# Optimization experiments

Measured on AMD Instinct MI355X. Metric: run time of the kernel, lower is better.

## Reference

```python
import jax, jax.numpy as jnp
import numpy as np

L = 2        # num_layers
B = 2        # batch
C = 256      # d_model
H = 8        # nhead
HD = C // H  # head_dim = 32
T = 16       # time_length
S = 512      # seq_length
DFF = 1024   # dim_feedforward
LIMIT = 25.0 # move_limit
EPS = 1e-5


def _xavier(key, shape):
    fan_in, fan_out = shape[-1], shape[-2]
    lim = np.sqrt(6.0 / (fan_in + fan_out)).astype(np.float32)
    return jax.random.uniform(key, shape, jnp.float32, -lim, lim)


def setup_inputs() -> dict:
    key = jax.random.key(0)
    ks = jax.random.split(key, 16)
    decoder = jax.random.normal(ks[0], (B, C, T, S), jnp.float32)
    encoder = jax.random.normal(ks[1], (B, C, T, S), jnp.float32)
    pos = jax.random.normal(ks[2], (B, C, T, S), jnp.float32)
    # coordinates in a 100-unit box so pairwise distances straddle move_limit=25
    coord = jax.random.uniform(ks[3], (B, T, S, 3), jnp.float32) * 100.0
    mask = jax.random.bernoulli(ks[4], 0.2, (B, T, S))  # True = padded key
    # per-layer params (stacked over L). qkv_proj is a groups=3 1x1 conv == three [C,C] mats.
    Wq = _xavier(ks[5], (L, C, C)); bq = jnp.zeros((L, C), jnp.float32)
    Wk = _xavier(ks[6], (L, C, C)); bk = jnp.zeros((L, C), jnp.float32)
    Wv = _xavier(ks[7], (L, C, C)); bv = jnp.zeros((L, C), jnp.float32)
    Wo = _xavier(ks[8], (L, C, C)); bo = jnp.zeros((L, C), jnp.float32)
    W1 = _xavier(ks[9], (L, DFF, C)); b1 = jnp.zeros((L, DFF), jnp.float32)
    W2 = _xavier(ks[10], (L, C, DFF)); b2 = jnp.zeros((L, C), jnp.float32)
    ln_g = jnp.ones((L, 3, C), jnp.float32)
    ln_b = jnp.zeros((L, 3, C), jnp.float32)
    return dict(decoder=decoder, encoder=encoder, pos=pos, coord=coord, mask=mask,
                Wq=Wq, bq=bq, Wk=Wk, bk=bk, Wv=Wv, bv=bv, Wo=Wo, bo=bo,
                W1=W1, b1=b1, W2=W2, b2=b2, ln_g=ln_g, ln_b=ln_b)


def _layernorm_c(x, g, b):
    # LayerNorm over channel dim of [B,C,T,S]
    m = jnp.mean(x, axis=1, keepdims=True)
    v = jnp.mean((x - m) ** 2, axis=1, keepdims=True)
    xn = (x - m) * jax.lax.rsqrt(v + EPS)
    return xn * g[None, :, None, None] + b[None, :, None, None]


def _proj(W, b, x):  # 1x1 conv == channel matmul on [B,C,T,S]
    return jnp.einsum('oc,bcts->bots', W, x) + b[None, :, None, None]


def _heads(x):  # [B,C,T,S] -> [B,H,T,S,HD]
    return x.reshape(B, H, HD, T, S).transpose(0, 1, 3, 4, 2)


def _dist_attn(x_q, x_k, x_v, coord, mask, Wq, bq, Wk, bk, Wv, bv, Wo, bo):
    q = _heads(_proj(Wq, bq, x_q))
    k = _heads(_proj(Wk, bk, x_k))
    v = _heads(_proj(Wv, bv, x_v))
    logits = jnp.einsum('bhtqd,bhtkd->bhtqk', q, k) / np.sqrt(HD).astype(np.float32)
    d2 = jnp.sum((coord[:, :, :, None, :] - coord[:, :, None, :, :]) ** 2, axis=-1)
    gate = (jnp.sqrt(d2) < LIMIT).astype(logits.dtype)  # [B,T,S,S]
    logits = logits * gate[:, None]
    logits = jnp.where(mask[:, None, :, None, :], jnp.asarray(-9e15, logits.dtype), logits)
    attn = jax.nn.softmax(logits, axis=-1)
    vals = jnp.einsum('bhtqk,bhtkd->bhtqd', attn, v)
    vals = vals.transpose(0, 1, 4, 2, 3).reshape(B, C, T, S)
    return _proj(Wo, bo, vals)


def _forward(decoder, encoder, pos, coord, mask,
             Wq, bq, Wk, bk, Wv, bv, Wo, bo, W1, b1, W2, b2, ln_g, ln_b):
    dec = decoder
    for i in range(L):
        a = lambda xq, xk, xv: _dist_attn(xq, xk, xv, coord, mask,
                                          Wq[i], bq[i], Wk[i], bk[i], Wv[i], bv[i], Wo[i], bo[i])
        # self-attention (queries/keys = norm(dec)+pos)
        src2 = _layernorm_c(dec, ln_g[i, 0], ln_b[i, 0])
        qk = src2 + pos
        dec = dec + a(qk, qk, src2)
        # second block: queries/keys from encoder+pos, values from norm(dec)
        # (the original uses self_attn weights here too)
        src2 = _layernorm_c(dec, ln_g[i, 1], ln_b[i, 1])
        qk = encoder + pos
        dec = dec + a(qk, qk, src2)
        # FFN
        src2 = _layernorm_c(dec, ln_g[i, 2], ln_b[i, 2])
        h = jax.nn.relu(jnp.einsum('fc,bcts->bfts', W1[i], src2) + b1[i][None, :, None, None])
        ff = jnp.einsum('cf,bfts->bcts', W2[i], h) + b2[i][None, :, None, None]
        dec = dec + ff
    return dec


def reference(decoder, encoder, pos, coord, mask,
              Wq, bq, Wk, bk, Wv, bv, Wo, bo, W1, b1, W2, b2, ln_g, ln_b):
    return _forward(decoder, encoder, pos, coord, mask,
                    Wq, bq, Wk, bk, Wv, bv, Wo, bo, W1, b1, W2, b2, ln_g, ln_b)
```

## Files before the change

### kernel.cpp

```cpp
#include <hip/hip_runtime.h>
#include <math.h>

#define L_ 2
#define B_ 2
#define C_ 256
#define H_ 8
#define HD_ 32
#define T_ 16
#define S_ 512
#define DFF_ 1024
#define NTS (T_*S_)
#define NELEM ((size_t)B_*C_*T_*S_)
#define QKM 512

typedef _Float16 half8v __attribute__((ext_vector_type(8)));
typedef _Float16 half4v __attribute__((ext_vector_type(4)));
typedef _Float16 half2v __attribute__((ext_vector_type(2)));
typedef float   float4v __attribute__((ext_vector_type(4)));

union h8u { half8v v; half2v h[4]; };

__global__ void prep_kernel(const float* __restrict__ Wq, const float* __restrict__ Wk,
                            const float* __restrict__ Wv, const float* __restrict__ Wo,
                            const float* __restrict__ W1, const float* __restrict__ W2,
                            const float* __restrict__ bq, const float* __restrict__ bk,
                            _Float16* __restrict__ whqk, _Float16* __restrict__ whv,
                            _Float16* __restrict__ who, _Float16* __restrict__ wh1,
                            _Float16* __restrict__ wh2, float* __restrict__ bqk) {
    int i = blockIdx.x * 256 + threadIdx.x;
    const int NQK = L_*QKM*C_;
    const int NCC = L_*C_*C_;
    const int NFC = L_*DFF_*C_;
    if (i < NQK) {
        int k = i & 255, m = (i >> 8) & 511, l = i >> 17;
        float v = (m < 256) ? Wq[((size_t)l*256 + m)*256 + k]
                            : Wk[((size_t)l*256 + (m-256))*256 + k];
        whqk[i] = (_Float16)v;
        return;
    }
    int j = i - NQK;
    if (j < NCC) { whv[j] = (_Float16)Wv[j]; return; }
    j -= NCC;
    if (j < NCC) { who[j] = (_Float16)Wo[j]; return; }
    j -= NCC;
    if (j < NFC) { wh1[j] = (_Float16)W1[j]; return; }
    j -= NFC;
    if (j < NFC) { wh2[j] = (_Float16)W2[j]; return; }
    j -= NFC;
    if (j < L_*QKM) {
        int c = j & 255, sel = (j >> 8) & 1, l = j >> 9;
        bqk[j] = sel ? bk[l*256 + c] : bq[l*256 + c];
    }
}

template<bool HASPOS>
__global__ __launch_bounds__(256) void ln_t(const float* __restrict__ x,
                                            const float* __restrict__ gam,
                                            const float* __restrict__ bet,
                                            const float* __restrict__ pos,
                                            _Float16* __restrict__ s2,
                                            _Float16* __restrict__ qk) {
    __shared__ float redS[8][32];
    __shared__ float redQ[8][32];
    __shared__ _Float16 tiles[(HASPOS ? 2 : 1) * 32 * 256];
    _Float16* t0 = tiles;
    _Float16* t1 = tiles + 32 * 256;
    int tid = threadIdx.x;
    int nl = tid & 31, cg = tid >> 5;
    int gpos = blockIdx.x * 32;
    int b = gpos >> 13, nb = gpos & 8191;
    const float* xb = x + (size_t)b * C_ * NTS + nb + nl;
    float xv[32], pv[HASPOS ? 32 : 1];
    float sum = 0.f, sq = 0.f;
    #pragma unroll
    for (int j = 0; j < 32; ++j) {
        float v = xb[(size_t)(cg * 32 + j) * NTS];
        xv[j] = v; sum += v; sq += v * v;
    }
    if (HASPOS) {
        const float* pb = pos + (size_t)b * C_ * NTS + nb + nl;
        #pragma unroll
        for (int j = 0; j < 32; ++j) pv[j] = pb[(size_t)(cg * 32 + j) * NTS];
    }
    redS[cg][nl] = sum; redQ[cg][nl] = sq;
    __syncthreads();
    float s = 0.f, q = 0.f;
    #pragma unroll
    for (int g = 0; g < 8; ++g) { s += redS[g][nl]; q += redQ[g][nl]; }
    float mean = s * (1.0f / C_);
    float var  = q * (1.0f / C_) - mean * mean;
    float rstd = rsqrtf(var + 1e-5f);
    #pragma unroll
    for (int jj = 0; jj < 4; ++jj) {
        half8v h0, h1;
        #pragma unroll
        for (int j2 = 0; j2 < 8; ++j2) {
            int j = jj * 8 + j2;
            int c = cg * 32 + j;
            float y = (xv[j] - mean) * rstd * gam[c] + bet[c];
            h0[j2] = (_Float16)y;
            if (HASPOS) h1[j2] = (_Float16)(y + pv[j]);
        }
        int cs = (cg * 4 + jj) ^ nl;
        *(half8v*)(t0 + nl * 256 + cs * 8) = h0;
        if (HASPOS) *(half8v*)(t1 + nl * 256 + cs * 8) = h1;
    }
    __syncthreads();
    #pragma unroll
    for (int it = 0; it < 4; ++it) {
        int chunk = tid + it * 256;
        int row = chunk >> 5, ch = chunk & 31;
        int cs = ch ^ row;
        half8v v0 = *(half8v*)(t0 + row * 256 + cs * 8);
        *(half8v*)(s2 + (size_t)(gpos + row) * C_ + ch * 8) = v0;
        if (HASPOS) {
            half8v v1 = *(half8v*)(t1 + row * 256 + cs * 8);
            *(half8v*)(qk + (size_t)(gpos + row) * C_ + ch * 8) = v1;
        }
    }
}

__global__ __launch_bounds__(256) void addt_kernel(const float* __restrict__ a,
                                                   const float* __restrict__ p,
                                                   _Float16* __restrict__ o) {
    __shared__ _Float16 t0[32 * 256];
    int tid = threadIdx.x;
    int nl = tid & 31, cg = tid >> 5;
    int gpos = blockIdx.x * 32;
    int b = gpos >> 13, nb = gpos & 8191;
    const float* ab = a + (size_t)b * C_ * NTS + nb + nl;
    const float* pb = p + (size_t)b * C_ * NTS + nb + nl;
    float av[32], pv[32];
    #pragma unroll
    for (int j = 0; j < 32; ++j) av[j] = ab[(size_t)(cg * 32 + j) * NTS];
    #pragma unroll
    for (int j = 0; j < 32; ++j) pv[j] = pb[(size_t)(cg * 32 + j) * NTS];
    #pragma unroll
    for (int jj = 0; jj < 4; ++jj) {
        half8v h0;
        #pragma unroll
        for (int j2 = 0; j2 < 8; ++j2) {
            int j = jj * 8 + j2;
            h0[j2] = (_Float16)(av[j] + pv[j]);
        }
        int cs = (cg * 4 + jj) ^ nl;
        *(half8v*)(t0 + nl * 256 + cs * 8) = h0;
    }
    __syncthreads();
    #pragma unroll
    for (int it = 0; it < 4; ++it) {
        int chunk = tid + it * 256;
        int row = chunk >> 5, ch = chunk & 31;
        half8v v0 = *(half8v*)(t0 + row * 256 + (ch ^ row) * 8);
        *(half8v*)(o + (size_t)(gpos + row) * C_ + ch * 8) = v0;
    }
}

template<int MODE>
__global__ __launch_bounds__(256) void gemm_mfma(const _Float16* __restrict__ W,
                                                 const float* __restrict__ bias,
                                                 const _Float16* __restrict__ X,
                                                 const float* __restrict__ src,
                                                 void* __restrict__ Yv, int M, int K) {
    __shared__ _Float16 As[128 * 32];
    __shared__ _Float16 Bs[128 * 32];
    int b  = blockIdx.z;
    int m0 = blockIdx.y * 128;
    int n0 = blockIdx.x * 128;
    const _Float16* Xb = X + (size_t)b * NTS * K;
    int tid = threadIdx.x;
    int wave = tid >> 6, lane = tid & 63;
    int wm = (wave >> 1) * 64, wn = (wave & 1) * 64;
    int r = lane & 15, g = lane >> 4;
    float4v acc[4][4];
    #pragma unroll
    for (int i = 0; i < 4; ++i)
        #pragma unroll
        for (int j = 0; j < 4; ++j) acc[i][j] = (float4v){0.f, 0.f, 0.f, 0.f};

    for (int k0 = 0; k0 < K; k0 += 32) {
        #pragma unroll
        for (int it = 0; it < 2; ++it) {
            int cbase = wave * 64 + it * 256;
            int rowbase = cbase >> 2;
            int row = rowbase + (lane >> 2);
            int ch = (lane & 3) ^ (row & 3);
            const _Float16* ga = W  + (size_t)(m0 + row) * K + k0 + ch * 8;
            const _Float16* gb = Xb + (size_t)(n0 + row) * K + k0 + ch * 8;
            __builtin_amdgcn_global_load_lds(
                (const __attribute__((address_space(1))) void*)ga,
                (__attribute__((address_space(3))) void*)(As + rowbase * 32), 16, 0, 0);
            __builtin_amdgcn_global_load_lds(
                (const __attribute__((address_space(1))) void*)gb,
                (__attribute__((address_space(3))) void*)(Bs + rowbase * 32), 16, 0, 0);
        }
        __syncthreads();
        half8v af[4], bf[4];
        #pragma unroll
        for (int mt = 0; mt < 4; ++mt) {
            int row = wm + mt * 16 + r;
            af[mt] = *(const half8v*)(As + row * 32 + ((g ^ (row & 3)) << 3));
        }
        #pragma unroll
        for (int nt = 0; nt < 4; ++nt) {
            int row = wn + nt * 16 + r;
            bf[nt] = *(const half8v*)(Bs + row * 32 + ((g ^ (row & 3)) << 3));
        }
        #pragma unroll
        for (int mt = 0; mt < 4; ++mt)
            #pragma unroll
            for (int nt = 0; nt < 4; ++nt)
                acc[mt][nt] = __builtin_amdgcn_mfma_f32_16x16x32_f16(af[mt], bf[nt], acc[mt][nt], 0, 0, 0);
        __syncthreads();
    }

    #pragma unroll
    for (int mt = 0; mt < 4; ++mt) {
        int m_base = m0 + wm + mt * 16 + g * 4;
        float bb[4];
        #pragma unroll
        for (int rr = 0; rr < 4; ++rr) bb[rr] = bias[m_base + rr];
        #pragma unroll
        for (int nt = 0; nt < 4; ++nt) {
            int n = n0 + wn + nt * 16 + r;
            if (MODE == 1) {
                float* Yd = (float*)Yv + (size_t)b * M * NTS;
                const float* Sd = src + (size_t)b * M * NTS;
                #pragma unroll
                for (int rr = 0; rr < 4; ++rr) {
                    size_t o = (size_t)(m_base + rr) * NTS + n;
                    Yd[o] = Sd[o] + acc[mt][nt][rr] + bb[rr];
                }
            } else {
                _Float16* Y = (_Float16*)Yv + (size_t)b * NTS * M;
                half4v hv;
                #pragma unroll
                for (int rr = 0; rr < 4; ++rr) {
                    float v = acc[mt][nt][rr] + bb[rr];
                    if (MODE == 2) v = fmaxf(v, 0.f);
                    hv[rr] = (_Float16)v;
                }
                *(half4v*)(Y + (size_t)n * M + m_base) = hv;
            }
        }
    }
}

__global__ __launch_bounds__(256) void gate_kernel(const float* __restrict__ coord,
                                                   const int* __restrict__ mask,
                                                   unsigned long long* __restrict__ gwb,
                                                   int* __restrict__ ucb,
                                                   unsigned long long* __restrict__ umb) {
    int wid  = blockIdx.x * 4 + (threadIdx.x >> 6);
    int lane = threadIdx.x & 63;
    int q  = wid & 511;
    int bt = wid >> 9;
    const float* cb = coord + (size_t)bt * S_ * 3;
    const int* mrow = mask + (size_t)bt * S_;
    float cq0 = cb[q*3+0], cq1 = cb[q*3+1], cq2 = cb[q*3+2];
    int ucnt = 0;
    for (int i = 0; i < 8; ++i) {
        int k = i * 64 + lane;
        float dx = cq0 - cb[k*3+0];
        float dy = cq1 - cb[k*3+1];
        float dz = cq2 - cb[k*3+2];
        bool near = (dx*dx + dy*dy + dz*dz) < 625.0f;
        bool um = (mrow[k] == 0);
        unsigned long long gm = __ballot(near && um);
        unsigned long long un = __ballot(um);
        if (lane == 0) {
            gwb[(size_t)wid*8 + i] = gm;
            ucnt += __popcll(un);
            if (q == 0) umb[bt*8 + i] = un;
        }
    }
    if (lane == 0) ucb[wid] = ucnt;
}

__global__ __launch_bounds__(256) void attn_kernel(
        const _Float16* __restrict__ qk, const _Float16* __restrict__ v,
        const unsigned long long* __restrict__ gwb, const int* __restrict__ ucb,
        const unsigned long long* __restrict__ umb, _Float16* __restrict__ out) {
    __shared__ _Float16 KV[S_ * 72];
    __shared__ float Upart[8][32];
    __shared__ float Ufin[HD_];
    int bid  = blockIdx.x;
    int half = bid & 1;
    int bht  = bid >> 1;
    int t = bht & (T_-1), h = (bht >> 4) & (H_-1), b = bht >> 7;
    int tid = threadIdx.x;
    int bt = b * T_ + t;
    const _Float16* kg = qk + ((size_t)bt * S_) * QKM + 256 + h * HD_;
    const _Float16* vg = v  + ((size_t)bt * S_) * C_  + h * HD_;

    #pragma unroll
    for (int it = 0; it < 8; ++it) {
        int c = tid + it * 256;
        int s = c >> 2, ch = c & 3;
        *(half8v*)(KV + s * 72 + ch * 8)      = *(const half8v*)(kg + (size_t)s * QKM + ch * 8);
        *(half8v*)(KV + s * 72 + 32 + ch * 8) = *(const half8v*)(vg + (size_t)s * C_ + ch * 8);
    }

    int qi = half * 256 + tid;
    h8u qa[4];
    {
        const half8v* qp = (const half8v*)(qk + ((size_t)bt * S_ + qi) * QKM + h * HD_);
        #pragma unroll
        for (int i = 0; i < 4; ++i) qa[i].v = qp[i];
    }
    __syncthreads();

    {
        int d = tid & 31, grp = tid >> 5;
        unsigned long long um = umb[bt*8 + grp];
        float s = 0.f;
        for (int kk = 0; kk < 64; ++kk)
            if ((um >> kk) & 1) s += (float)KV[(grp*64 + kk) * 72 + 32 + d];
        Upart[grp][d] = s;
    }
    __syncthreads();
    if (tid < HD_) {
        float s = 0.f;
        #pragma unroll
        for (int gp = 0; gp < 8; ++gp) s += Upart[gp][tid];
        Ufin[tid] = s;
    }
    __syncthreads();

    const unsigned long long* gw8 = gwb + ((size_t)bt * S_ + qi) * 8;
    float O[HD_];
    #pragma unroll
    for (int d = 0; d < HD_; ++d) O[d] = 0.f;
    float l = (float)ucb[(size_t)bt * S_ + qi];

    for (int w = 0; w < 8; ++w) {
        unsigned long long gw = gw8[w];
        while (gw) {
            int j = __builtin_ctzll(gw);
            gw &= gw - 1;
            const _Float16* row = KV + (w * 64 + j) * 72;
            h8u k0, k1, k2, k3;
            k0.v = *(const half8v*)(row);
            k1.v = *(const half8v*)(row + 8);
            k2.v = *(const half8v*)(row + 16);
            k3.v = *(const half8v*)(row + 24);
            float s = 0.f;
            #pragma unroll
            for (int i = 0; i < 4; ++i) {
                s = __builtin_amdgcn_fdot2(k0.h[i], qa[0].h[i], s, false);
                s = __builtin_amdgcn_fdot2(k1.h[i], qa[1].h[i], s, false);
                s = __builtin_amdgcn_fdot2(k2.h[i], qa[2].h[i], s, false);
                s = __builtin_amdgcn_fdot2(k3.h[i], qa[3].h[i], s, false);
            }
            s *= 0.17677669529663687f;
            float e = __expf(fminf(s, 80.f));
            float em1 = e - 1.f;
            l += em1;
            half8v v0 = *(const half8v*)(row + 32);
            half8v v1 = *(const half8v*)(row + 40);
            half8v v2 = *(const half8v*)(row + 48);
            half8v v3 = *(const half8v*)(row + 56);
            #pragma unroll
            for (int d = 0; d < 8; ++d) {
                O[d]      = fmaf((float)v0[d], em1, O[d]);
                O[d + 8]  = fmaf((float)v1[d], em1, O[d + 8]);
                O[d + 16] = fmaf((float)v2[d], em1, O[d + 16]);
                O[d + 24] = fmaf((float)v3[d], em1, O[d + 24]);
            }
        }
    }
    float invl = 1.0f / l;
    _Float16* orow = out + ((size_t)bt * S_ + qi) * C_ + h * HD_;
    #pragma unroll
    for (int c0 = 0; c0 < 4; ++c0) {
        half8v hv;
        #pragma unroll
        for (int j = 0; j < 8; ++j)
            hv[j] = (_Float16)((O[c0*8+j] + Ufin[c0*8+j]) * invl);
        *(half8v*)(orow + c0 * 8) = hv;
    }
}

extern "C" void kernel_launch(void* const* d_in, const int* in_sizes, int n_in,
                              void* d_out, int out_size, void* d_ws, size_t ws_size,
                              hipStream_t stream) {
    const float* decoder = (const float*)d_in[0];
    const float* encoder = (const float*)d_in[1];
    const float* pos     = (const float*)d_in[2];
    const float* coord   = (const float*)d_in[3];
    const int*   mask    = (const int*)d_in[4];
    const float* Wq = (const float*)d_in[5],  *bq = (const float*)d_in[6];
    const float* Wk = (const float*)d_in[7],  *bk = (const float*)d_in[8];
    const float* Wv = (const float*)d_in[9],  *bv = (const float*)d_in[10];
    const float* Wo = (const float*)d_in[11], *bo = (const float*)d_in[12];
    const float* W1 = (const float*)d_in[13], *b1 = (const float*)d_in[14];
    const float* W2 = (const float*)d_in[15], *b2 = (const float*)d_in[16];
    const float* ln_g = (const float*)d_in[17], *ln_b = (const float*)d_in[18];

    float* dec = (float*)d_out;

    size_t actsz = (size_t)B_ * NTS * C_;
    _Float16* qkT  = (_Float16*)d_ws;
    _Float16* qkT2 = qkT + actsz;
    _Float16* vT   = qkT2 + 2*actsz;
    _Float16* s2T  = vT + actsz;
    _Float16* hT   = qkT;
    _Float16* whqk = s2T + actsz;
    _Float16* whv  = whqk + (size_t)L_*QKM*C_;
    _Float16* who  = whv + (size_t)L_*C_*C_;
    _Float16* wh1  = who + (size_t)L_*C_*C_;
    _Float16* wh2  = wh1 + (size_t)L_*DFF_*C_;
    float* bqk = (float*)(wh2 + (size_t)L_*C_*DFF_);
    unsigned long long* gwb = (unsigned long long*)(bqk + L_*QKM);
    int* ucb = (int*)(gwb + (size_t)B_*T_*S_*8);
    unsigned long long* umb = (unsigned long long*)(ucb + (size_t)B_*T_*S_);

    dim3 gGridQK(NTS/128, QKM/128, B_);
    dim3 gGridC(NTS/128, C_/128, B_);
    dim3 gGridF(NTS/128, DFF_/128, B_);
    dim3 lnGrid(B_ * NTS / 32);
    dim3 attnGrid(B_ * H_ * T_ * 2);
    dim3 gateGrid(B_ * T_ * S_ / 4);
    dim3 prepGrid(6148);

    gate_kernel<<<gateGrid, 256, 0, stream>>>(coord, mask, gwb, ucb, umb);
    prep_kernel<<<prepGrid, 256, 0, stream>>>(Wq, Wk, Wv, Wo, W1, W2, bq, bk,
                                              whqk, whv, who, wh1, wh2, bqk);

    for (int l = 0; l < L_; ++l) {
        const _Float16* whqk_l = whqk + (size_t)l*QKM*C_; const float* bqk_l = bqk + l*QKM;
        const _Float16* whv_l = whv + (size_t)l*C_*C_;  const float* bv_l = bv + l*C_;
        const _Float16* who_l = who + (size_t)l*C_*C_;  const float* bo_l = bo + l*C_;
        const _Float16* wh1_l = wh1 + (size_t)l*DFF_*C_; const float* b1_l = b1 + l*DFF_;
        const _Float16* wh2_l = wh2 + (size_t)l*C_*DFF_; const float* b2_l = b2 + l*C_;
        const float* g0 = ln_g + ((size_t)l*3 + 0)*C_; const float* e0 = ln_b + ((size_t)l*3 + 0)*C_;
        const float* g1 = ln_g + ((size_t)l*3 + 1)*C_; const float* e1 = ln_b + ((size_t)l*3 + 1)*C_;
        const float* g2 = ln_g + ((size_t)l*3 + 2)*C_; const float* e2 = ln_b + ((size_t)l*3 + 2)*C_;

        const float* x0 = (l == 0) ? decoder : dec;
        const float* r0 = (l == 0) ? decoder : dec;

        ln_t<true><<<lnGrid, 256, 0, stream>>>(x0, g0, e0, pos, s2T, qkT);
        gemm_mfma<0><<<gGridQK, 256, 0, stream>>>(whqk_l, bqk_l, qkT, nullptr, qkT2, QKM, C_);
        gemm_mfma<0><<<gGridC, 256, 0, stream>>>(whv_l, bv_l, s2T, nullptr, vT, C_, C_);
        attn_kernel<<<attnGrid, 256, 0, stream>>>(qkT2, vT, gwb, ucb, umb, s2T);
        gemm_mfma<1><<<gGridC, 256, 0, stream>>>(who_l, bo_l, s2T, r0, dec, C_, C_);

        ln_t<false><<<lnGrid, 256, 0, stream>>>(dec, g1, e1, nullptr, s2T, nullptr);
        addt_kernel<<<lnGrid, 256, 0, stream>>>(encoder, pos, qkT);
        gemm_mfma<0><<<gGridQK, 256, 0, stream>>>(whqk_l, bqk_l, qkT, nullptr, qkT2, QKM, C_);
        gemm_mfma<0><<<gGridC, 256, 0, stream>>>(whv_l, bv_l, s2T, nullptr, vT, C_, C_);
        attn_kernel<<<attnGrid, 256, 0, stream>>>(qkT2, vT, gwb, ucb, umb, s2T);
        gemm_mfma<1><<<gGridC, 256, 0, stream>>>(who_l, bo_l, s2T, dec, dec, C_, C_);

        ln_t<false><<<lnGrid, 256, 0, stream>>>(dec, g2, e2, nullptr, s2T, nullptr);
        gemm_mfma<2><<<gGridF, 256, 0, stream>>>(wh1_l, b1_l, s2T, nullptr, hT, DFF_, C_);
        gemm_mfma<1><<<gGridC, 256, 0, stream>>>(wh2_l, b2_l, hT, dec, dec, C_, DFF_);
    }
}
```

Baseline: 569.3 us.

## Fuse QK/V projections and residual GEMMs with following LayerNorm

Merges the QK and V projection GEMMs into one launch by splitting grid rows between the two weight sets. Fuses the output-projection and FFN2 GEMMs with the residual add and the next LayerNorm: each block covers all 256 channels for 64 columns, so the channel statistics are reduced inside the block. Also precomputes encoder+pos once instead of per layer. This removes separate LayerNorm and add kernels and their extra activation round trips. The cost is less parallelism per fused GEMM, since the grid now has fewer, larger blocks, plus a larger workspace.

```diff
diff --git a/kernel.cpp b/kernel.cpp
--- a/kernel.cpp
+++ b/kernel.cpp
@@ -242,6 +242,217 @@
                 }
                 *(half4v*)(Y + (size_t)n * M + m_base) = hv;
             }
+        }
+    }
+}
+
+__global__ __launch_bounds__(256) void gemm_qkv(
+        const _Float16* __restrict__ Wqk, const float* __restrict__ bqk,
+        const _Float16* __restrict__ Xqk, _Float16* __restrict__ Yqk,
+        const _Float16* __restrict__ Wv, const float* __restrict__ bv,
+        const _Float16* __restrict__ Xv, _Float16* __restrict__ Yv) {
+    __shared__ _Float16 As[128 * 32];
+    __shared__ _Float16 Bs[128 * 32];
+    const _Float16 *W, *X; const float* bias; _Float16* Y; int M, m0;
+    if (blockIdx.y < 4) { W = Wqk; bias = bqk; X = Xqk; Y = Yqk; M = QKM; m0 = blockIdx.y * 128; }
+    else                { W = Wv;  bias = bv;  X = Xv;  Y = Yv;  M = C_;  m0 = (blockIdx.y - 4) * 128; }
+    const int K = C_;
+    int b  = blockIdx.z;
+    int n0 = blockIdx.x * 128;
+    const _Float16* Xb = X + (size_t)b * NTS * K;
+    int tid = threadIdx.x;
+    int wave = tid >> 6, lane = tid & 63;
+    int wm = (wave >> 1) * 64, wn = (wave & 1) * 64;
+    int r = lane & 15, g = lane >> 4;
+    float4v acc[4][4];
+    #pragma unroll
+    for (int i = 0; i < 4; ++i)
+        #pragma unroll
+        for (int j = 0; j < 4; ++j) acc[i][j] = (float4v){0.f, 0.f, 0.f, 0.f};
+
+    for (int k0 = 0; k0 < K; k0 += 32) {
+        #pragma unroll
+        for (int it = 0; it < 2; ++it) {
+            int cbase = wave * 64 + it * 256;
+            int rowbase = cbase >> 2;
+            int row = rowbase + (lane >> 2);
+            int ch = (lane & 3) ^ (row & 3);
+            const _Float16* ga = W  + (size_t)(m0 + row) * K + k0 + ch * 8;
+            const _Float16* gb = Xb + (size_t)(n0 + row) * K + k0 + ch * 8;
+            __builtin_amdgcn_global_load_lds(
+                (const __attribute__((address_space(1))) void*)ga,
+                (__attribute__((address_space(3))) void*)(As + rowbase * 32), 16, 0, 0);
+            __builtin_amdgcn_global_load_lds(
+                (const __attribute__((address_space(1))) void*)gb,
+                (__attribute__((address_space(3))) void*)(Bs + rowbase * 32), 16, 0, 0);
+        }
+        __syncthreads();
+        half8v af[4], bf[4];
+        #pragma unroll
+        for (int mt = 0; mt < 4; ++mt) {
+            int row = wm + mt * 16 + r;
+            af[mt] = *(const half8v*)(As + row * 32 + ((g ^ (row & 3)) << 3));
+        }
+        #pragma unroll
+        for (int nt = 0; nt < 4; ++nt) {
+            int row = wn + nt * 16 + r;
+            bf[nt] = *(const half8v*)(Bs + row * 32 + ((g ^ (row & 3)) << 3));
+        }
+        #pragma unroll
+        for (int mt = 0; mt < 4; ++mt)
+            #pragma unroll
+            for (int nt = 0; nt < 4; ++nt)
+                acc[mt][nt] = __builtin_amdgcn_mfma_f32_16x16x32_f16(af[mt], bf[nt], acc[mt][nt], 0, 0, 0);
+        __syncthreads();
+    }
+    #pragma unroll
+    for (int mt = 0; mt < 4; ++mt) {
+        int m_base = m0 + wm + mt * 16 + g * 4;
+        float bb[4];
+        #pragma unroll
+        for (int rr = 0; rr < 4; ++rr) bb[rr] = bias[m_base + rr];
+        #pragma unroll
+        for (int nt = 0; nt < 4; ++nt) {
+            int n = n0 + wn + nt * 16 + r;
+            half4v hv;
+            #pragma unroll
+            for (int rr = 0; rr < 4; ++rr)
+                hv[rr] = (_Float16)(acc[mt][nt][rr] + bb[rr]);
+            *(half4v*)(Y + ((size_t)b * NTS + n) * M + m_base) = hv;
+        }
+    }
+}
+
+template<bool POS>
+__global__ __launch_bounds__(256) void gemm_res_ln(
+        const _Float16* __restrict__ W, const float* __restrict__ bias,
+        const _Float16* __restrict__ X, const float* __restrict__ src,
+        float* __restrict__ dec, const float* __restrict__ gam,
+        const float* __restrict__ bet, const float* __restrict__ pos,
+        _Float16* __restrict__ s2, _Float16* __restrict__ qk, int K) {
+    __shared__ _Float16 As[256 * 32];
+    __shared__ _Float16 Bs[64 * 32];
+    __shared__ float sumS[4][64], sumQ[4][64];
+    __shared__ float meanL[64], rstdL[64];
+    int b  = blockIdx.z;
+    int n0 = blockIdx.x * 64;
+    const _Float16* Xb = X + (size_t)b * NTS * K;
+    int tid = threadIdx.x;
+    int wave = tid >> 6, lane = tid & 63;
+    int wm = wave * 64;
+    int r = lane & 15, g = lane >> 4;
+    float4v acc[4][4];
+    #pragma unroll
+    for (int i = 0; i < 4; ++i)
+        #pragma unroll
+        for (int j = 0; j < 4; ++j) acc[i][j] = (float4v){0.f, 0.f, 0.f, 0.f};
+
+    for (int k0 = 0; k0 < K; k0 += 32) {
+        #pragma unroll
+        for (int it = 0; it < 4; ++it) {
+            int cbase = wave * 64 + it * 256;
+            int rowbase = cbase >> 2;
+            int row = rowbase + (lane >> 2);
+            int ch = (lane & 3) ^ (row & 3);
+            const _Float16* ga = W + (size_t)row * K + k0 + ch * 8;
+            __builtin_amdgcn_global_load_lds(
+                (const __attribute__((address_space(1))) void*)ga,
+                (__attribute__((address_space(3))) void*)(As + rowbase * 32), 16, 0, 0);
+        }
+        {
+            int cbase = wave * 64;
+            int rowbase = cbase >> 2;
+            int row = rowbase + (lane >> 2);
+            int ch = (lane & 3) ^ (row & 3);
+            const _Float16* gb = Xb + (size_t)(n0 + row) * K + k0 + ch * 8;
+            __builtin_amdgcn_global_load_lds(
+                (const __attribute__((address_space(1))) void*)gb,
+                (__attribute__((address_space(3))) void*)(Bs + rowbase * 32), 16, 0, 0);
+        }
+        __syncthreads();
+        half8v af[4], bf[4];
+        #pragma unroll
+        for (int mt = 0; mt < 4; ++mt) {
+            int row = wm + mt * 16 + r;
+            af[mt] = *(const half8v*)(As + row * 32 + ((g ^ (row & 3)) << 3));
+        }
+        #pragma unroll
+        for (int nt = 0; nt < 4; ++nt) {
+            int row = nt * 16 + r;
+            bf[nt] = *(const half8v*)(Bs + row * 32 + ((g ^ (row & 3)) << 3));
+        }
+        #pragma unroll
+        for (int mt = 0; mt < 4; ++mt)
+            #pragma unroll
+            for (int nt = 0; nt < 4; ++nt)
+                acc[mt][nt] = __builtin_amdgcn_mfma_f32_16x16x32_f16(af[mt], bf[nt], acc[mt][nt], 0, 0, 0);
+        __syncthreads();
+    }
+
+    const float* Sd = src + (size_t)b * C_ * NTS;
+    float* Dd = dec + (size_t)b * C_ * NTS;
+    #pragma unroll
+    for (int mt = 0; mt < 4; ++mt) {
+        int mb = wm + mt * 16 + g * 4;
+        float bb[4];
+        #pragma unroll
+        for (int rr = 0; rr < 4; ++rr) bb[rr] = bias[mb + rr];
+        #pragma unroll
+        for (int nt = 0; nt < 4; ++nt) {
+            int n = n0 + nt * 16 + r;
+            #pragma unroll
+            for (int rr = 0; rr < 4; ++rr) {
+                size_t o = (size_t)(mb + rr) * NTS + n;
+                float v = Sd[o] + acc[mt][nt][rr] + bb[rr];
+                acc[mt][nt][rr] = v;
+                Dd[o] = v;
+            }
+        }
+    }
+    #pragma unroll
+    for (int nt = 0; nt < 4; ++nt) {
+        float ps = 0.f, pq = 0.f;
+        #pragma unroll
+        for (int mt = 0; mt < 4; ++mt)
+            #pragma unroll
+            for (int rr = 0; rr < 4; ++rr) {
+                float v = acc[mt][nt][rr];
+                ps += v; pq += v * v;
+            }
+        ps += __shfl_xor(ps, 16, 64); pq += __shfl_xor(pq, 16, 64);
+        ps += __shfl_xor(ps, 32, 64); pq += __shfl_xor(pq, 32, 64);
+        if (g == 0) { sumS[wave][nt * 16 + r] = ps; sumQ[wave][nt * 16 + r] = pq; }
+    }
+    __syncthreads();
+    if (tid < 64) {
+        float s = sumS[0][tid] + sumS[1][tid] + sumS[2][tid] + sumS[3][tid];
+        float q = sumQ[0][tid] + sumQ[1][tid] + sumQ[2][tid] + sumQ[3][tid];
+        float mean = s * (1.0f / C_);
+        float var  = q * (1.0f / C_) - mean * mean;
+        meanL[tid] = mean;
+        rstdL[tid] = rsqrtf(var + 1e-5f);
+    }
+    __syncthreads();
+    const float* Pb = POS ? pos + (size_t)b * C_ * NTS : nullptr;
+    #pragma unroll
+    for (int mt = 0; mt < 4; ++mt) {
+        int mb = wm + mt * 16 + g * 4;
+        float gm[4], be[4];
+        #pragma unroll
+        for (int rr = 0; rr < 4; ++rr) { gm[rr] = gam[mb + rr]; be[rr] = bet[mb + rr]; }
+        #pragma unroll
+        for (int nt = 0; nt < 4; ++nt) {
+            int n = n0 + nt * 16 + r;
+            float mean = meanL[nt * 16 + r], rstd = rstdL[nt * 16 + r];
+            half4v hv, hq;
+            #pragma unroll
+            for (int rr = 0; rr < 4; ++rr) {
+                float y = (acc[mt][nt][rr] - mean) * rstd * gm[rr] + be[rr];
+                hv[rr] = (_Float16)y;
+                if (POS) hq[rr] = (_Float16)(y + Pb[(size_t)(mb + rr) * NTS + n]);
+            }
+            *(half4v*)(s2 + ((size_t)b * NTS + n) * C_ + mb) = hv;
+            if (POS) *(half4v*)(qk + ((size_t)b * NTS + n) * C_ + mb) = hq;
         }
     }
 }
@@ -404,8 +615,10 @@
     _Float16* qkT2 = qkT + actsz;
     _Float16* vT   = qkT2 + 2*actsz;
     _Float16* s2T  = vT + actsz;
-    _Float16* hT   = qkT;
-    _Float16* whqk = s2T + actsz;
+    _Float16* aT   = s2T + actsz;
+    _Float16* encT = aT + actsz;
+    _Float16* hT   = encT + actsz;
+    _Float16* whqk = hT + 4*actsz;
     _Float16* whv  = whqk + (size_t)L_*QKM*C_;
     _Float16* who  = whv + (size_t)L_*C_*C_;
     _Float16* wh1  = who + (size_t)L_*C_*C_;
@@ -415,9 +628,10 @@
     int* ucb = (int*)(gwb + (size_t)B_*T_*S_*8);
     unsigned long long* umb = (unsigned long long*)(ucb + (size_t)B_*T_*S_);
 
-    dim3 gGridQK(NTS/128, QKM/128, B_);
+    dim3 gGridQKV(NTS/128, 6, B_);
     dim3 gGridC(NTS/128, C_/128, B_);
     dim3 gGridF(NTS/128, DFF_/128, B_);
+    dim3 gGridRL(NTS/64, 1, B_);
     dim3 lnGrid(B_ * NTS / 32);
     dim3 attnGrid(B_ * H_ * T_ * 2);
     dim3 gateGrid(B_ * T_ * S_ / 4);
@@ -426,6 +640,7 @@
     gate_kernel<<<gateGrid, 256, 0, stream>>>(coord, mask, gwb, ucb, umb);
     prep_kernel<<<prepGrid, 256, 0, stream>>>(Wq, Wk, Wv, Wo, W1, W2, bq, bk,
                                               whqk, whv, who, wh1, wh2, bqk);
+    addt_kernel<<<lnGrid, 256, 0, stream>>>(encoder, pos, encT);
 
     for (int l = 0; l < L_; ++l) {
         const _Float16* whqk_l = whqk + (size_t)l*QKM*C_; const float* bqk_l = bqk + l*QKM;
@@ -437,24 +652,28 @@
         const float* g1 = ln_g + ((size_t)l*3 + 1)*C_; const float* e1 = ln_b + ((size_t)l*3 + 1)*C_;
         const float* g2 = ln_g + ((size_t)l*3 + 2)*C_; const float* e2 = ln_b + ((size_t)l*3 + 2)*C_;
 
-        const float* x0 = (l == 0) ? decoder : dec;
-        const float* r0 = (l == 0) ? decoder : dec;
-
-        ln_t<true><<<lnGrid, 256, 0, stream>>>(x0, g0, e0, pos, s2T, qkT);
-        gemm_mfma<0><<<gGridQK, 256, 0, stream>>>(whqk_l, bqk_l, qkT, nullptr, qkT2, QKM, C_);
-        gemm_mfma<0><<<gGridC, 256, 0, stream>>>(whv_l, bv_l, s2T, nullptr, vT, C_, C_);
-        attn_kernel<<<attnGrid, 256, 0, stream>>>(qkT2, vT, gwb, ucb, umb, s2T);
-        gemm_mfma<1><<<gGridC, 256, 0, stream>>>(who_l, bo_l, s2T, r0, dec, C_, C_);
-
-        ln_t<false><<<lnGrid, 256, 0, stream>>>(dec, g1, e1, nullptr, s2T, nullptr);
-        addt_kernel<<<lnGrid, 256, 0, stream>>>(encoder, pos, qkT);
-        gemm_mfma<0><<<gGridQK, 256, 0, stream>>>(whqk_l, bqk_l, qkT, nullptr, qkT2, QKM, C_);
-        gemm_mfma<0><<<gGridC, 256, 0, stream>>>(whv_l, bv_l, s2T, nullptr, vT, C_, C_);
-        attn_kernel<<<attnGrid, 256, 0, stream>>>(qkT2, vT, gwb, ucb, umb, s2T);
-        gemm_mfma<1><<<gGridC, 256, 0, stream>>>(who_l, bo_l, s2T, dec, dec, C_, C_);
-
-        ln_t<false><<<lnGrid, 256, 0, stream>>>(dec, g2, e2, nullptr, s2T, nullptr);
+        if (l == 0)
+            ln_t<true><<<lnGrid, 256, 0, stream>>>(decoder, g0, e0, pos, s2T, qkT);
+        gemm_qkv<<<gGridQKV, 256, 0, stream>>>(whqk_l, bqk_l, qkT, qkT2,
+                                               whv_l, bv_l, s2T, vT);
+        attn_kernel<<<attnGrid, 256, 0, stream>>>(qkT2, vT, gwb, ucb, umb, aT);
+        gemm_res_ln<false><<<gGridRL, 256, 0, stream>>>(who_l, bo_l, aT,
+                (l == 0) ? decoder : dec, dec, g1, e1, nullptr, s2T, nullptr, C_);
+
+        gemm_qkv<<<gGridQKV, 256, 0, stream>>>(whqk_l, bqk_l, encT, qkT2,
+                                               whv_l, bv_l, s2T, vT);
+        attn_kernel<<<attnGrid, 256, 0, stream>>>(qkT2, vT, gwb, ucb, umb, aT);
+        gemm_res_ln<false><<<gGridRL, 256, 0, stream>>>(who_l, bo_l, aT,
+                dec, dec, g2, e2, nullptr, s2T, nullptr, C_);
+
         gemm_mfma<2><<<gGridF, 256, 0, stream>>>(wh1_l, b1_l, s2T, nullptr, hT, DFF_, C_);
-        gemm_mfma<1><<<gGridC, 256, 0, stream>>>(wh2_l, b2_l, hT, dec, dec, C_, DFF_);
-    }
-}
+        if (l + 1 < L_) {
+            const float* g0n = ln_g + ((size_t)(l+1)*3 + 0)*C_;
+            const float* e0n = ln_b + ((size_t)(l+1)*3 + 0)*C_;
+            gemm_res_ln<true><<<gGridRL, 256, 0, stream>>>(wh2_l, b2_l, hT,
+                    dec, dec, g0n, e0n, pos, s2T, qkT, DFF_);
+        } else {
+            gemm_mfma<1><<<gGridC, 256, 0, stream>>>(wh2_l, b2_l, hT, dec, dec, C_, DFF_);
+        }
+    }
+}
```

After: 535.0 us. -6.0%, faster.
